# Kernel tuning notes

Measured on AMD Instinct MI355X. Metric: run time of the kernel, lower is better.

The kernel has to match this reference:

```python
import math
import jax, jax.numpy as jnp
import numpy as np

N, D = 16384, 1024


def setup_inputs() -> dict:
    key = jax.random.key(0)
    k1, k2 = jax.random.split(key)
    return {
        "image_embeddings_aligned": jax.random.normal(k1, (N, D), dtype=jnp.float32),
        "text_embeddings_aligned": jax.random.normal(k2, (N, D), dtype=jnp.float32),
        "logit_scale": jnp.asarray(math.log(20.0), dtype=jnp.float32),  # stored as log(init)
        "logit_bias": jnp.asarray(-10.0, dtype=jnp.float32),
    }


def _l2_normalize(x, eps=1e-12):
    # matches F.normalize(p=2, dim=-1)
    n = jnp.linalg.norm(x, axis=-1, keepdims=True)
    return x / jnp.maximum(n, eps)


def reference(image_embeddings_aligned, text_embeddings_aligned, logit_scale, logit_bias):
    img = _l2_normalize(image_embeddings_aligned)
    txt = _l2_normalize(text_embeddings_aligned)
    # [N, N] pairwise logits
    logits = jnp.exp(logit_scale) * jnp.einsum("nd,md->nm", img, txt) + logit_bias
    n = logits.shape[0]
    labels = 2.0 * jnp.eye(n, dtype=logits.dtype) - 1.0  # +1 on diagonal, -1 off
    loss_matrix = jax.nn.log_sigmoid(labels * logits)
    siglip_loss = -jnp.mean(loss_matrix)  # total_loss (structure_lambda == 0)
    return siglip_loss
```

## Files before the change

### kernel.cpp

```cpp
#include <hip/hip_runtime.h>

#define NROWS 16384
#define DIM   1024
#define QSCALE 32.0f
#define E8M0S  0x7A7A7A7Au

typedef int    v4i    __attribute__((ext_vector_type(4)));
typedef int    v8i    __attribute__((ext_vector_type(8)));
typedef float  f32x16 __attribute__((ext_vector_type(16)));

__device__ __forceinline__ void glds16(const void* g, void* l) {
    __builtin_amdgcn_global_load_lds(
        (const __attribute__((address_space(1))) void*)g,
        (__attribute__((address_space(3))) void*)l,
        16, 0, 0);
}

__device__ __forceinline__ float fexp2(float x) {
#if __has_builtin(__builtin_amdgcn_exp2f)
    return __builtin_amdgcn_exp2f(x);
#else
    return exp2f(x);
#endif
}
__device__ __forceinline__ float flog2(float x) {
#if __has_builtin(__builtin_amdgcn_logf)
    return __builtin_amdgcn_logf(x);
#else
    return log2f(x);
#endif
}

__device__ __forceinline__ unsigned fp4_nib(float y) {
    unsigned s = (__float_as_uint(y) >> 31) << 3;
    float a = fminf(fabsf(y), 6.0f);
    unsigned c = (unsigned)(a >= 0.25f) + (unsigned)(a >= 0.75f) +
                 (unsigned)(a >= 1.25f) + (unsigned)(a >= 1.75f) +
                 (unsigned)(a >= 2.5f)  + (unsigned)(a >= 3.5f)  +
                 (unsigned)(a >= 5.0f);
    return c | s;
}

__global__ __launch_bounds__(256) void norm_fused(
    const float* __restrict__ img,
    const float* __restrict__ txt,
    unsigned char* __restrict__ imgQ,
    unsigned char* __restrict__ txtQ,
    const float* __restrict__ lscale,
    const float* __restrict__ lbias,
    float* __restrict__ diagPart) {
    const int t    = threadIdx.x;
    const int lane = t & 63;
    const int wave = t >> 6;
    const int gw   = blockIdx.x * 4 + wave;
    const float sc   = __expf(lscale[0]);
    const float bias = lbias[0];

    for (int row = gw; row < NROWS; row += 8192) {
        const float4* pi = (const float4*)(img + (size_t)row * DIM);
        const float4* pt = (const float4*)(txt + (size_t)row * DIM);
        float4 vi[4], vt[4];
        float ssi = 0.0f, sst = 0.0f, dot = 0.0f;
        #pragma unroll
        for (int j = 0; j < 4; ++j) {
            vi[j] = pi[lane + 64 * j];
            vt[j] = pt[lane + 64 * j];
            ssi += vi[j].x*vi[j].x + vi[j].y*vi[j].y + vi[j].z*vi[j].z + vi[j].w*vi[j].w;
            sst += vt[j].x*vt[j].x + vt[j].y*vt[j].y + vt[j].z*vt[j].z + vt[j].w*vt[j].w;
            dot += vi[j].x*vt[j].x + vi[j].y*vt[j].y + vi[j].z*vt[j].z + vi[j].w*vt[j].w;
        }
        #pragma unroll
        for (int off = 1; off < 64; off <<= 1) {
            ssi += __shfl_xor(ssi, off, 64);
            sst += __shfl_xor(sst, off, 64);
            dot += __shfl_xor(dot, off, 64);
        }
        const float ii = 1.0f / fmaxf(sqrtf(ssi), 1e-12f);
        const float it = 1.0f / fmaxf(sqrtf(sst), 1e-12f);
        if (lane == 0) diagPart[row] = -fmaf(sc, dot * ii * it, bias);

        const float qi = ii * QSCALE, qt = it * QSCALE;
        ushort* oi = (ushort*)(imgQ + (size_t)row * 512);
        ushort* ot = (ushort*)(txtQ + (size_t)row * 512);
        #pragma unroll
        for (int j = 0; j < 4; ++j) {
            unsigned p = fp4_nib(vi[j].x * qi)        | (fp4_nib(vi[j].y * qi) << 4) |
                         (fp4_nib(vi[j].z * qi) << 8) | (fp4_nib(vi[j].w * qi) << 12);
            unsigned q = fp4_nib(vt[j].x * qt)        | (fp4_nib(vt[j].y * qt) << 4) |
                         (fp4_nib(vt[j].z * qt) << 8) | (fp4_nib(vt[j].w * qt) << 12);
            oi[lane + 64 * j] = (ushort)p;
            ot[lane + 64 * j] = (ushort)q;
        }
    }
}

__global__ __launch_bounds__(256, 2) void siglip_gemm(
    const unsigned char* __restrict__ A,
    const unsigned char* __restrict__ B,
    const float* __restrict__ lscale,
    const float* __restrict__ lbias,
    float* __restrict__ gemmPart)
{
    __shared__ unsigned char sA[256 * 128];
    __shared__ unsigned char sB[128 * 128];
    __shared__ float wred[4];

    const int t    = threadIdx.x;
    const int lane = t & 63;
    const int wave = t >> 6;
    const int wr   = wave >> 1;
    const int wc   = wave & 1;
    const int r31  = lane & 31;
    const int h    = lane >> 5;
    const int xr   = (r31 & 7) ^ ((r31 >> 4) & 1);

    const int GRID_N = NROWS / 128;
    const int GM = 16;
    int b = blockIdx.x;
    int group = b / (GM * GRID_N);
    int ing   = b % (GM * GRID_N);
    int brow  = group * GM + (ing % GM);
    int bcol  = ing / GM;

    const size_t aBase = (size_t)brow * 256;
    const size_t bBase = (size_t)bcol * 128;

    const int srow = lane >> 3;
    const int c0   = (lane & 7) ^ srow;
    const int d01  = (c0 & 1) ? -16 : 16;

    const unsigned char* aP = A + (size_t)(aBase + wave * 64 + srow) * 512 + c0 * 16;
    const unsigned char* bP = B + (size_t)(bBase + wave * 32 + srow) * 512 + c0 * 16;
    char* lA0 = ((char*)sA) + wave * 8192;
    char* lB0 = ((char*)sB) + wave * 4096;

    int rbA[4], rbB[2];
    #pragma unroll
    for (int i = 0; i < 4; ++i) rbA[i] = (wr * 128 + i * 32 + r31) * 128;
    #pragma unroll
    for (int i = 0; i < 2; ++i) rbB[i] = (wc * 64 + i * 32 + r31) * 128;

    f32x16 acc[4][2] = {};

    for (int k = 0; k < 4; ++k) {
        __syncthreads();
        #pragma unroll
        for (int j = 0; j < 8; ++j) {
            const int tog = ((j >> 1) & 1) ? d01 : 0;
            glds16(aP + j * 8 * 512 + tog, lA0 + j * 1024);
        }
        #pragma unroll
        for (int j = 0; j < 4; ++j) {
            const int tog = ((j >> 1) & 1) ? d01 : 0;
            glds16(bP + j * 8 * 512 + tog, lB0 + j * 1024);
        }
        aP += 128;
        bP += 128;
        __syncthreads();

        #pragma unroll
        for (int ks = 0; ks < 4; ++ks) {
            const int s = ((ks * 2 + h) ^ xr) * 16;
            v8i af[4], bf[2];
            #pragma unroll
            for (int i = 0; i < 4; ++i) {
                v4i v = *(const v4i*)(sA + rbA[i] + s);
                af[i] = __builtin_shufflevector(v, v, 0, 1, 2, 3, -1, -1, -1, -1);
            }
            #pragma unroll
            for (int i = 0; i < 2; ++i) {
                v4i v = *(const v4i*)(sB + rbB[i] + s);
                bf[i] = __builtin_shufflevector(v, v, 0, 1, 2, 3, -1, -1, -1, -1);
            }
            #pragma unroll
            for (int mi = 0; mi < 4; ++mi)
                #pragma unroll
                for (int ni = 0; ni < 2; ++ni)
                    acc[mi][ni] = __builtin_amdgcn_mfma_scale_f32_32x32x64_f8f6f4(
                        af[mi], bf[ni], acc[mi][ni],
                        4, 4,
                        0, (int)E8M0S,
                        0, (int)E8M0S);
        }
    }

    const float l2e   = 1.44269504088896341f;
    const float scale = __expf(lscale[0]);
    const float aCo   = scale * l2e;
    const float bCo   = lbias[0] * l2e;
    float local = 0.0f;
    #pragma unroll
    for (int mi = 0; mi < 4; ++mi)
        #pragma unroll
        for (int ni = 0; ni < 2; ++ni)
            #pragma unroll
            for (int r = 0; r < 16; r += 4) {
                float e0 = fexp2(fmaf(aCo, acc[mi][ni][r + 0], bCo));
                float e1 = fexp2(fmaf(aCo, acc[mi][ni][r + 1], bCo));
                float e2 = fexp2(fmaf(aCo, acc[mi][ni][r + 2], bCo));
                float e3 = fexp2(fmaf(aCo, acc[mi][ni][r + 3], bCo));
                float p  = ((1.0f + e0) * (1.0f + e1)) *
                           ((1.0f + e2) * (1.0f + e3));
                local += flog2(p);
            }

    #pragma unroll
    for (int off = 32; off > 0; off >>= 1) local += __shfl_down(local, off, 64);
    if (lane == 0) wred[wave] = local;
    __syncthreads();
    if (t == 0)
        gemmPart[blockIdx.x] =
            (wred[0] + wred[1] + wred[2] + wred[3]) * 0.69314718055994531f;
}

__global__ __launch_bounds__(1024) void finalize_kernel(
    const float* __restrict__ parts, float* __restrict__ out) {
    __shared__ float wr[16];
    const int t    = threadIdx.x;
    const int lane = t & 63;
    const int wave = t >> 6;
    const float4* p4 = (const float4*)parts;
    float s = 0.0f;
    for (int i = t; i < 6144; i += 1024) {
        float4 v = p4[i];
        s += v.x + v.y + v.z + v.w;
    }
    #pragma unroll
    for (int off = 32; off > 0; off >>= 1) s += __shfl_down(s, off, 64);
    if (lane == 0) wr[wave] = s;
    __syncthreads();
    if (t == 0) {
        float tot = 0.0f;
        #pragma unroll
        for (int i = 0; i < 16; ++i) tot += wr[i];
        out[0] = tot / 268435456.0f;
    }
}

extern "C" void kernel_launch(void* const* d_in, const int* in_sizes, int n_in,
                              void* d_out, int out_size, void* d_ws, size_t ws_size,
                              hipStream_t stream) {
    const float* img    = (const float*)d_in[0];
    const float* txt    = (const float*)d_in[1];
    const float* lscale = (const float*)d_in[2];
    const float* lbias  = (const float*)d_in[3];
    float* out = (float*)d_out;

    char* ws = (char*)d_ws;
    unsigned char* imgQ = (unsigned char*)ws;
    unsigned char* txtQ = (unsigned char*)(ws + (size_t)NROWS * 512);
    float* parts   = (float*)(ws + (size_t)2 * NROWS * 512);
    float* diagPart = parts;
    float* gemmPart = parts + NROWS;

    norm_fused<<<2048, 256, 0, stream>>>(img, txt, imgQ, txtQ, lscale, lbias, diagPart);
    siglip_gemm<<<dim3((NROWS / 256) * (NROWS / 128)), 256, 0, stream>>>(
        imgQ, txtQ, lscale, lbias, gemmPart);
    finalize_kernel<<<1, 1024, 0, stream>>>(parts, out);
}
```

Before: 310.0 us.

## Pre-pack FP4 operands in MFMA fragment order and load directly from global

The quantization kernel now writes FP4 embeddings in a fragment-major layout, grouping 32 rows into a contiguous panel so each lane's MFMA operand is one 16-byte chunk. The GEMM drops its LDS staging, barriers and swizzling, and each wave loads its A/B fragments straight from global memory into registers. This removes LDS traffic and synchronization, but operand reuse across waves now depends on L1/L2 caching, and there is no software prefetch or double buffering. The occupancy hint in the launch bounds is also loosened.

```diff
diff --git a/kernel.cpp b/kernel.cpp
--- a/kernel.cpp
+++ b/kernel.cpp
@@ -4,17 +4,11 @@
 #define DIM   1024
 #define QSCALE 32.0f
 #define E8M0S  0x7A7A7A7Au
+#define PSTRIDE 16384
 
 typedef int    v4i    __attribute__((ext_vector_type(4)));
 typedef int    v8i    __attribute__((ext_vector_type(8)));
 typedef float  f32x16 __attribute__((ext_vector_type(16)));
-
-__device__ __forceinline__ void glds16(const void* g, void* l) {
-    __builtin_amdgcn_global_load_lds(
-        (const __attribute__((address_space(1))) void*)g,
-        (__attribute__((address_space(3))) void*)l,
-        16, 0, 0);
-}
 
 __device__ __forceinline__ float fexp2(float x) {
 #if __has_builtin(__builtin_amdgcn_exp2f)
@@ -80,29 +74,30 @@
         if (lane == 0) diagPart[row] = -fmaf(sc, dot * ii * it, bias);
 
         const float qi = ii * QSCALE, qt = it * QSCALE;
-        ushort* oi = (ushort*)(imgQ + (size_t)row * 512);
-        ushort* ot = (ushort*)(txtQ + (size_t)row * 512);
+        unsigned char* qib = imgQ + (size_t)(row >> 5) * PSTRIDE + (row & 31) * 16
+                           + (lane & 7) * 2;
+        unsigned char* qtb = txtQ + (size_t)(row >> 5) * PSTRIDE + (row & 31) * 16
+                           + (lane & 7) * 2;
+        const int cbase = (lane >> 3) * 512;
         #pragma unroll
         for (int j = 0; j < 4; ++j) {
             unsigned p = fp4_nib(vi[j].x * qi)        | (fp4_nib(vi[j].y * qi) << 4) |
                          (fp4_nib(vi[j].z * qi) << 8) | (fp4_nib(vi[j].w * qi) << 12);
             unsigned q = fp4_nib(vt[j].x * qt)        | (fp4_nib(vt[j].y * qt) << 4) |
                          (fp4_nib(vt[j].z * qt) << 8) | (fp4_nib(vt[j].w * qt) << 12);
-            oi[lane + 64 * j] = (ushort)p;
-            ot[lane + 64 * j] = (ushort)q;
+            *(ushort*)(qib + cbase + j * (8 * 512)) = (ushort)p;
+            *(ushort*)(qtb + cbase + j * (8 * 512)) = (ushort)q;
         }
     }
 }
 
-__global__ __launch_bounds__(256, 2) void siglip_gemm(
+__global__ __launch_bounds__(256) void siglip_gemm(
     const unsigned char* __restrict__ A,
     const unsigned char* __restrict__ B,
     const float* __restrict__ lscale,
     const float* __restrict__ lbias,
     float* __restrict__ gemmPart)
 {
-    __shared__ unsigned char sA[256 * 128];
-    __shared__ unsigned char sB[128 * 128];
     __shared__ float wred[4];
 
     const int t    = threadIdx.x;
@@ -110,9 +105,6 @@
     const int wave = t >> 6;
     const int wr   = wave >> 1;
     const int wc   = wave & 1;
-    const int r31  = lane & 31;
-    const int h    = lane >> 5;
-    const int xr   = (r31 & 7) ^ ((r31 >> 4) & 1);
 
     const int GRID_N = NROWS / 128;
     const int GM = 16;
@@ -122,66 +114,42 @@
     int brow  = group * GM + (ing % GM);
     int bcol  = ing / GM;
 
-    const size_t aBase = (size_t)brow * 256;
-    const size_t bBase = (size_t)bcol * 128;
-
-    const int srow = lane >> 3;
-    const int c0   = (lane & 7) ^ srow;
-    const int d01  = (c0 & 1) ? -16 : 16;
-
-    const unsigned char* aP = A + (size_t)(aBase + wave * 64 + srow) * 512 + c0 * 16;
-    const unsigned char* bP = B + (size_t)(bBase + wave * 32 + srow) * 512 + c0 * 16;
-    char* lA0 = ((char*)sA) + wave * 8192;
-    char* lB0 = ((char*)sB) + wave * 4096;
-
-    int rbA[4], rbB[2];
-    #pragma unroll
-    for (int i = 0; i < 4; ++i) rbA[i] = (wr * 128 + i * 32 + r31) * 128;
-    #pragma unroll
-    for (int i = 0; i < 2; ++i) rbB[i] = (wc * 64 + i * 32 + r31) * 128;
+    const unsigned char* aF[4];
+    const unsigned char* bF[2];
+    #pragma unroll
+    for (int i = 0; i < 4; ++i)
+        aF[i] = A + (size_t)(brow * 8 + wr * 4 + i) * PSTRIDE + lane * 16;
+    #pragma unroll
+    for (int i = 0; i < 2; ++i)
+        bF[i] = B + (size_t)(bcol * 4 + wc * 2 + i) * PSTRIDE + lane * 16;
 
     f32x16 acc[4][2] = {};
 
-    for (int k = 0; k < 4; ++k) {
-        __syncthreads();
-        #pragma unroll
-        for (int j = 0; j < 8; ++j) {
-            const int tog = ((j >> 1) & 1) ? d01 : 0;
-            glds16(aP + j * 8 * 512 + tog, lA0 + j * 1024);
-        }
-        #pragma unroll
-        for (int j = 0; j < 4; ++j) {
-            const int tog = ((j >> 1) & 1) ? d01 : 0;
-            glds16(bP + j * 8 * 512 + tog, lB0 + j * 1024);
-        }
-        aP += 128;
-        bP += 128;
-        __syncthreads();
-
-        #pragma unroll
-        for (int ks = 0; ks < 4; ++ks) {
-            const int s = ((ks * 2 + h) ^ xr) * 16;
-            v8i af[4], bf[2];
+    #pragma unroll 4
+    for (int c2 = 0; c2 < 16; ++c2) {
+        const int off = c2 * 1024;
+        v4i a0 = *(const v4i*)(aF[0] + off);
+        v4i a1 = *(const v4i*)(aF[1] + off);
+        v4i a2 = *(const v4i*)(aF[2] + off);
+        v4i a3 = *(const v4i*)(aF[3] + off);
+        v4i b0 = *(const v4i*)(bF[0] + off);
+        v4i b1 = *(const v4i*)(bF[1] + off);
+        v8i af[4], bf[2];
+        af[0] = __builtin_shufflevector(a0, a0, 0, 1, 2, 3, -1, -1, -1, -1);
+        af[1] = __builtin_shufflevector(a1, a1, 0, 1, 2, 3, -1, -1, -1, -1);
+        af[2] = __builtin_shufflevector(a2, a2, 0, 1, 2, 3, -1, -1, -1, -1);
+        af[3] = __builtin_shufflevector(a3, a3, 0, 1, 2, 3, -1, -1, -1, -1);
+        bf[0] = __builtin_shufflevector(b0, b0, 0, 1, 2, 3, -1, -1, -1, -1);
+        bf[1] = __builtin_shufflevector(b1, b1, 0, 1, 2, 3, -1, -1, -1, -1);
+        #pragma unroll
+        for (int mi = 0; mi < 4; ++mi)
             #pragma unroll
-            for (int i = 0; i < 4; ++i) {
-                v4i v = *(const v4i*)(sA + rbA[i] + s);
-                af[i] = __builtin_shufflevector(v, v, 0, 1, 2, 3, -1, -1, -1, -1);
-            }
-            #pragma unroll
-            for (int i = 0; i < 2; ++i) {
-                v4i v = *(const v4i*)(sB + rbB[i] + s);
-                bf[i] = __builtin_shufflevector(v, v, 0, 1, 2, 3, -1, -1, -1, -1);
-            }
-            #pragma unroll
-            for (int mi = 0; mi < 4; ++mi)
-                #pragma unroll
-                for (int ni = 0; ni < 2; ++ni)
-                    acc[mi][ni] = __builtin_amdgcn_mfma_scale_f32_32x32x64_f8f6f4(
-                        af[mi], bf[ni], acc[mi][ni],
-                        4, 4,
-                        0, (int)E8M0S,
-                        0, (int)E8M0S);
-        }
+            for (int ni = 0; ni < 2; ++ni)
+                acc[mi][ni] = __builtin_amdgcn_mfma_scale_f32_32x32x64_f8f6f4(
+                    af[mi], bf[ni], acc[mi][ni],
+                    4, 4,
+                    0, (int)E8M0S,
+                    0, (int)E8M0S);
     }
 
     const float l2e   = 1.44269504088896341f;
```

After: 561.0 us. 1.81x slower.
